# Kernel optimization log

Measured on AMD Instinct MI355X. Metric: run time of the kernel, lower is better.

Reference implementation:

```python
import jax, jax.numpy as jnp
import numpy as np

B, S, T, D = 4, 2, 1024, 512
H = 8
HD = D // H
EPS = 1e-6
LN_EPS = 1e-5


def setup_inputs() -> dict:
    key = jax.random.key(0)
    ks = jax.random.split(key, 12)
    def lin(k, fan_in, shape):
        bound = 1.0 / np.sqrt(fan_in)
        return jax.random.uniform(k, shape, jnp.float32, -bound, bound)
    return {
        "hidden_states": jax.random.normal(ks[0], (B, S, T, D), jnp.float32),
        "Wq": lin(ks[1], D, (D, D)), "bq": lin(ks[2], D, (D,)),
        "Wk": lin(ks[3], D, (D, D)), "bk": lin(ks[4], D, (D,)),
        "Wv": lin(ks[5], D, (D, D)), "bv": lin(ks[6], D, (D,)),
        "Wo": lin(ks[7], D, (D, D)), "bo": lin(ks[8], D, (D,)),
        "ln_g": jnp.ones((S, D), jnp.float32),
        "ln_b": jnp.zeros((S, D), jnp.float32),
        "gate_alpha": jnp.full((S,), 0.01, jnp.float32),
    }


def _heads(x):
    # [B,T,D] -> [B,H,T,HD]
    return x.reshape(B, T, H, HD).transpose(0, 2, 1, 3)


def _layernorm(x, g, b):
    mu = jnp.mean(x, axis=-1, keepdims=True)
    var = jnp.var(x, axis=-1, keepdims=True)
    return (x - mu) * jax.lax.rsqrt(var + LN_EPS) * g + b


def reference(hidden_states, Wq, bq, Wk, bk, Wv, bv, Wo, bo, ln_g, ln_b, gate_alpha):
    h1, h2 = hidden_states[:, 0], hidden_states[:, 1]  # [B,T,D]
    proj = lambda x, W, b: jnp.einsum('btd,ed->bte', x, W) + b
    Q1, K1, V1 = _heads(proj(h1, Wq, bq)), _heads(proj(h1, Wk, bk)), _heads(proj(h1, Wv, bv))
    Q2, K2, V2 = _heads(proj(h2, Wq, bq)), _heads(proj(h2, Wk, bk)), _heads(proj(h2, Wv, bv))
    scale = 1.0 / np.sqrt(HD)
    L12 = jnp.einsum('bhqd,bhkd->bhqk', Q1, K2) * scale
    L21 = jnp.einsum('bhqd,bhkd->bhqk', Q2, K1) * scale
    S12 = jax.nn.softmax(L12, axis=-1)
    S21 = jax.nn.softmax(L21, axis=-1)
    M = S12 + S21 + EPS
    A12 = S12 / M
    A21 = S21 / M
    H1 = jnp.einsum('bhqk,bhkd->bhqd', A12, V2).transpose(0, 2, 1, 3).reshape(B, T, D)
    H2 = jnp.einsum('bhqk,bhkd->bhqd', A21, V1).transpose(0, 2, 1, 3).reshape(B, T, D)
    H1 = _layernorm(jnp.einsum('btd,ed->bte', H1, Wo) + bo, ln_g[0], ln_b[0])
    H2 = _layernorm(jnp.einsum('btd,ed->bte', H2, Wo) + bo, ln_g[1], ln_b[1])
    attn = jnp.stack([H1, H2], axis=1)  # [B,2,T,D]
    return hidden_states + attn * gate_alpha[None, :, None, None]
```

## Files before the change

### kernel.cpp

```cpp
#include <hip/hip_runtime.h>

#define DEVI __device__ __forceinline__

typedef __bf16 v8bf __attribute__((ext_vector_type(8)));
typedef float  v4f  __attribute__((ext_vector_type(4)));
typedef short  v4s  __attribute__((ext_vector_type(4)));

DEVI unsigned short f2bf(float f) {
  unsigned u = __builtin_bit_cast(unsigned, f);
  u += 0x7fffu + ((u >> 16) & 1u);
  return (unsigned short)(u >> 16);
}
DEVI v4f MFMA32(v8bf a, v8bf b, v4f c) {
  return __builtin_amdgcn_mfma_f32_16x16x32_bf16(a, b, c, 0, 0, 0);
}
DEVI v8bf ldfrag(const unsigned short* p) {
  return __builtin_bit_cast(v8bf, *(const uint4*)p);
}
DEVI v4s ld4s(const unsigned short* p) {
  return __builtin_bit_cast(v4s, *(const uint2*)p);
}
DEVI unsigned pkbf(float lo, float hi) {
  unsigned a = __builtin_bit_cast(unsigned, hi) + 0x8000u;
  unsigned b = __builtin_bit_cast(unsigned, lo) + 0x8000u;
  return __builtin_amdgcn_perm(a, b, 0x07060302u);
}
DEVI float lo2f(unsigned u) { return __builtin_bit_cast(float, u << 16); }
DEVI float hi2f(unsigned u) { return __builtin_bit_cast(float, u & 0xffff0000u); }

DEVI void drain_vmem() { asm volatile("s_waitcnt vmcnt(0)" ::: "memory"); }

#if __has_builtin(__builtin_amdgcn_exp2f)
DEVI float fexp2(float x) { return __builtin_amdgcn_exp2f(x); }
#else
DEVI float fexp2(float x) { return exp2f(x); }
#endif

#if __has_builtin(__builtin_amdgcn_mfma_f32_16x16x16bf16_1k)
#define HAVE_MFMA16 1
DEVI v4f MFMA16(v4s a, v4s b, v4f c) {
  return __builtin_amdgcn_mfma_f32_16x16x16bf16_1k(a, b, c, 0, 0, 0);
}
#else
#define HAVE_MFMA16 0
#endif

#if __has_builtin(__builtin_amdgcn_global_load_lds)
DEVI void g2l(const unsigned short* g, unsigned short* l) {
  __builtin_amdgcn_global_load_lds(
      (const __attribute__((address_space(1))) unsigned int*)g,
      (__attribute__((address_space(3))) unsigned int*)l, 16, 0, 0);
}
#else
DEVI void g2l(const unsigned short* g, unsigned short* l) {
  *(uint4*)((char*)l + (threadIdx.x & 63) * 16) = *(const uint4*)g;
}
#endif

__global__ __launch_bounds__(256) void convert_kernel(
    const float* __restrict__ X, const float* __restrict__ Wq,
    const float* __restrict__ Wk, const float* __restrict__ Wv,
    const float* __restrict__ Wo, unsigned short* __restrict__ dst)
{
  int t = blockIdx.x * 256 + threadIdx.x;
  int idx = t * 4;
  const float* src;
  if (idx < 4194304) {
    src = X + idx;
  } else {
    int u = idx - 4194304;
    int w = u >> 18;
    const float* W = (w == 0) ? Wq : (w == 1) ? Wk : (w == 2) ? Wv : Wo;
    src = W + (u & 262143);
  }
  float4 f = *(const float4*)src;
  uint2 o;
  o.x = pkbf(f.x, f.y);
  o.y = pkbf(f.z, f.w);
  *(uint2*)&dst[idx] = o;
}

template<int OUTM, int BM>
__global__ __launch_bounds__(256) void gemm_bt(
    const unsigned short* __restrict__ A,
    const unsigned short* __restrict__ W0, const unsigned short* __restrict__ W1,
    const unsigned short* __restrict__ W2,
    const float* __restrict__ b0, const float* __restrict__ b1, const float* __restrict__ b2,
    void* __restrict__ C0, void* __restrict__ C1, void* __restrict__ C2)
{
  const int K = 512, N = 512;
  const int MI = BM / 32;
  const int PER = (BM / 8 + 16) / 4;
  __shared__ unsigned short sAB[2][(BM + 128) * 64];

  const int gx = gridDim.x, gy = gridDim.y;
  const int nwg = gx * gy * gridDim.z;
  const int lin = (blockIdx.z * gy + blockIdx.y) * gx + blockIdx.x;
  const int wsw = (lin & 7) * (nwg >> 3) + (lin >> 3);
  const int bx = wsw % gx, by = (wsw / gx) % gy;
  const int z = wsw / (gx * gy);

  const unsigned short* W = (z == 0) ? W0 : (z == 1) ? W1 : W2;
  const float* bias = (z == 0) ? b0 : (z == 1) ? b1 : b2;
  void* C = (z == 0) ? C0 : (z == 1) ? C1 : C2;

  const int tid = threadIdx.x;
  const int lane = tid & 63, wave = tid >> 6;
  const int l15 = lane & 15, quad = lane >> 4, swl = l15 & 7;
  const int lrow = lane >> 3;
  const int lc8 = ((lane & 7) ^ (lrow & 7)) * 8;
  const int wm = (wave >> 1) * (BM / 2), wn = (wave & 1) * 64;
  const int mbase = by * BM, nbase = bx * 128;

  const unsigned short* gsrc[PER];
  int loff[PER];
#pragma unroll
  for (int t = 0; t < PER; t++) {
    int c = wave * PER + t;
    loff[t] = c * 512;
    if (c < BM / 8) gsrc[t] = A + (size_t)(mbase + c * 8 + lrow) * K + lc8;
    else            gsrc[t] = W + (size_t)(nbase + (c - BM / 8) * 8 + lrow) * K + lc8;
  }

  v4f acc[MI][4] = {};

#pragma unroll
  for (int t = 0; t < PER; t++) g2l(gsrc[t], &sAB[0][loff[t]]);

  for (int kt = 0; kt < K / 64; kt++) {
    drain_vmem();
    __syncthreads();
    if (kt < K / 64 - 1) {
#pragma unroll
      for (int t = 0; t < PER; t++)
        g2l(gsrc[t] + (kt + 1) * 64, &sAB[(kt + 1) & 1][loff[t]]);
    }
    const int bu = kt & 1;
#pragma unroll
    for (int s = 0; s < 2; s++) {
      v8bf af[MI], bf[4];
#pragma unroll
      for (int i = 0; i < MI; i++)
        af[i] = ldfrag(&sAB[bu][(wm + i * 16 + l15) * 64 + ((s * 4 + quad) ^ swl) * 8]);
#pragma unroll
      for (int j = 0; j < 4; j++)
        bf[j] = ldfrag(&sAB[bu][(BM + wn + j * 16 + l15) * 64 + ((s * 4 + quad) ^ swl) * 8]);
#pragma unroll
      for (int i = 0; i < MI; i++)
#pragma unroll
        for (int j = 0; j < 4; j++)
          acc[i][j] = MFMA32(af[i], bf[j], acc[i][j]);
    }
  }

  if (OUTM == 0 && BM == 128 && z == 2) {
    const int TP = 136;
    unsigned short* T = &sAB[0][0];
    __syncthreads();
#pragma unroll
    for (int i = 0; i < MI; i++)
#pragma unroll
      for (int j = 0; j < 4; j++) {
        int tp = wm + i * 16 + quad * 4;
        int c  = wn + j * 16 + l15;
        int col = nbase + c;
        float v[4];
#pragma unroll
        for (int r = 0; r < 4; r++) v[r] = acc[i][j][r] + bias[col];
        uint2 o;
        o.x = pkbf(v[0], v[1]);
        o.y = pkbf(v[2], v[3]);
        *(uint2*)&T[c * TP + tp] = o;
      }
    __syncthreads();
    const int bs = mbase >> 10, tbase = mbase & 1023;
    const int hh0 = nbase >> 6;
#pragma unroll
    for (int it = 0; it < 8; it++) {
      int rh = wave * 32 + it * 4 + quad;
      uint4 d = *(const uint4*)&T[rh * TP + l15 * 8];
      int rowIdx = (bs * 8 + hh0 + (rh >> 6)) * 64 + (rh & 63);
      *(uint4*)&((unsigned short*)C)[(size_t)rowIdx * 1024 + tbase + l15 * 8] = d;
    }
  } else {
#pragma unroll
    for (int i = 0; i < MI; i++)
#pragma unroll
      for (int j = 0; j < 4; j++) {
        int row0 = mbase + wm + i * 16 + quad * 4;
        int col = nbase + wn + j * 16 + l15;
        float v[4];
#pragma unroll
        for (int r = 0; r < 4; r++) v[r] = acc[i][j][r] + bias[col];
        if (OUTM == 1) {
#pragma unroll
          for (int r = 0; r < 4; r++) ((float*)C)[(size_t)(row0 + r) * N + col] = v[r];
        } else if (z == 2) {
          int bs = row0 >> 10, t0 = row0 & 1023;
          int hh = col >> 6, hd = col & 63;
          uint2 o;
          o.x = pkbf(v[0], v[1]);
          o.y = pkbf(v[2], v[3]);
          *(uint2*)&((unsigned short*)C)[(size_t)((bs * 8 + hh) * 64 + hd) * 1024 + t0] = o;
        } else {
#pragma unroll
          for (int r = 0; r < 4; r++)
            ((unsigned short*)C)[(size_t)(row0 + r) * N + col] = f2bf(v[r]);
        }
      }
  }
}

__global__ __launch_bounds__(256, 4) void attn_a(
    const unsigned short* __restrict__ Qg, const unsigned short* __restrict__ Kg,
    float* __restrict__ Lws)
{
  __shared__ unsigned short sK[2][2][64][64];

  const int pair = blockIdx.x & 31;
  const int b = pair >> 3, h = pair & 7;
  const int qt = (blockIdx.x >> 5) & 15;
  const int kh = blockIdx.x >> 9;
  const int tid = threadIdx.x;
  const int lane = tid & 63, wave = tid >> 6;
  const int l15 = lane & 15, quad = lane >> 4, swl = l15 & 7;
  const int lrow = lane >> 3;
  const int lc8 = ((lane & 7) ^ (lrow & 7)) * 8;
  const int qbase = qt * 64 + wave * 16;
  const float S2 = 0.125f * 1.44269504f;

  const unsigned short* kgp[2];
#pragma unroll
  for (int st = 0; st < 2; st++)
    kgp[st] = Kg + (size_t)((b * 2 + st) * 1024) * 512 + h * 64;

  v8bf qf[2][2];
#pragma unroll
  for (int d = 0; d < 2; d++)
#pragma unroll
    for (int s = 0; s < 2; s++) {
      int qrow = (b * 2 + d) * 1024 + qbase + l15;
      qf[d][s] = ldfrag(&Qg[(size_t)qrow * 512 + h * 64 + s * 32 + quad * 8]);
    }

  const unsigned short* gA[4];
  unsigned short* lA[2][4];
#pragma unroll
  for (int t = 0; t < 4; t++) {
    int c = wave * 4 + t;
    gA[t] = kgp[c >> 3] + (size_t)((c & 7) * 8 + lrow) * 512 + lc8
            + (size_t)kh * 262144;
    lA[0][t] = &sK[0][c >> 3][(c & 7) * 8][0];
    lA[1][t] = &sK[1][c >> 3][(c & 7) * 8][0];
  }

  float lacc[2] = {0.f, 0.f};
#pragma unroll
  for (int t = 0; t < 4; t++) g2l(gA[t], lA[0][t]);

  for (int kt = 0; kt < 8; kt++) {
    drain_vmem();
    __syncthreads();
    if (kt < 7) {
#pragma unroll
      for (int t = 0; t < 4; t++)
        g2l(gA[t] + (size_t)(kt + 1) * 32768, lA[(kt + 1) & 1][t]);
    }
    const int bu = kt & 1;
    v4f acc[2][4] = {};
#pragma unroll
    for (int s = 0; s < 2; s++)
#pragma unroll
      for (int d = 0; d < 2; d++)
#pragma unroll
        for (int j = 0; j < 4; j++) {
          v8bf kf = ldfrag(&sK[bu][1 - d][j * 16 + l15][((s * 4 + quad) ^ swl) * 8]);
          acc[d][j] = MFMA32(kf, qf[d][s], acc[d][j]);
        }
#pragma unroll
    for (int d = 0; d < 2; d++)
#pragma unroll
      for (int j = 0; j < 4; j++)
#pragma unroll
        for (int r = 0; r < 4; r++)
          lacc[d] += fexp2(acc[d][j][r] * S2);
  }

  float lv[2];
#pragma unroll
  for (int d = 0; d < 2; d++) {
    float v = lacc[d];
    v += __shfl_xor(v, 16);
    v += __shfl_xor(v, 32);
    lv[d] = v;
  }
  if (quad == 0) {
#pragma unroll
    for (int d = 0; d < 2; d++) {
      int qrow = (b * 2 + d) * 1024 + qbase + l15;
      Lws[(size_t)qrow * 2 + kh] = lv[d];
    }
  }
}

__global__ __launch_bounds__(256, 2) void attn_b(
    const unsigned short* __restrict__ Qg, const unsigned short* __restrict__ Kg,
    const unsigned short* __restrict__ VTg, const float* __restrict__ Lws,
    unsigned short* __restrict__ Hc)
{
  __shared__ unsigned short sK[2][2][64][64];
  __shared__ unsigned short sV[2][2][64][64];

  const int pair = blockIdx.x & 31;
  const int b = pair >> 3, h = pair & 7;
  const int qt = blockIdx.x >> 5;
  const int tid = threadIdx.x;
  const int lane = tid & 63, wave = tid >> 6;
  const int l15 = lane & 15, quad = lane >> 4, swl = l15 & 7;
  const int lrow = lane >> 3;
  const int lc8 = ((lane & 7) ^ (lrow & 7)) * 8;
  const int qbase = qt * 64 + wave * 16;
  const float S2 = 0.125f * 1.44269504f;

  const unsigned short* kgp[2];
  const unsigned short* vgp[2];
#pragma unroll
  for (int st = 0; st < 2; st++) {
    kgp[st] = Kg + (size_t)((b * 2 + st) * 1024) * 512 + h * 64;
    vgp[st] = VTg + (size_t)(((b * 2 + st) * 8 + h) * 64) * 1024;
  }

  v8bf qf[2][2];
#pragma unroll
  for (int d = 0; d < 2; d++)
#pragma unroll
    for (int s = 0; s < 2; s++) {
      int qrow = (b * 2 + d) * 1024 + qbase + l15;
      qf[d][s] = ldfrag(&Qg[(size_t)qrow * 512 + h * 64 + s * 32 + quad * 8]);
    }

  float ll[2];
#pragma unroll
  for (int d = 0; d < 2; d++) {
    int qrow = (b * 2 + d) * 1024 + qbase + l15;
    float2 p = *(const float2*)&Lws[(size_t)qrow * 2];
    ll[d] = __log2f(p.x + p.y);
  }
  const float dll = ll[0] - ll[1];

  v4f oacc[2][4] = {};
  {
    const unsigned short* gB[8];
    unsigned short* lB[2][8];
    size_t stp[8];
#pragma unroll
    for (int t = 0; t < 8; t++) {
      int c = wave * 8 + t;
      if (c < 16) {
        gB[t] = kgp[c >> 3] + (size_t)((c & 7) * 8 + lrow) * 512 + lc8;
        stp[t] = 32768;
        lB[0][t] = &sK[0][c >> 3][(c & 7) * 8][0];
        lB[1][t] = &sK[1][c >> 3][(c & 7) * 8][0];
      } else {
        int cv = c - 16;
        gB[t] = vgp[cv >> 3] + (size_t)((cv & 7) * 8 + lrow) * 1024 + lc8;
        stp[t] = 64;
        lB[0][t] = &sV[0][cv >> 3][(cv & 7) * 8][0];
        lB[1][t] = &sV[1][cv >> 3][(cv & 7) * 8][0];
      }
    }
#pragma unroll
    for (int t = 0; t < 8; t++) g2l(gB[t], lB[0][t]);

    for (int kt = 0; kt < 16; kt++) {
      drain_vmem();
      __syncthreads();
      if (kt < 15) {
#pragma unroll
        for (int t = 0; t < 8; t++)
          g2l(gB[t] + (size_t)(kt + 1) * stp[t], lB[(kt + 1) & 1][t]);
      }
      const int bu = kt & 1;

      v4f acc[2][4] = {};
#pragma unroll
      for (int s = 0; s < 2; s++)
#pragma unroll
        for (int d = 0; d < 2; d++)
#pragma unroll
          for (int j = 0; j < 4; j++) {
            v8bf kf = ldfrag(&sK[bu][1 - d][j * 16 + l15][((s * 4 + quad) ^ swl) * 8]);
            acc[d][j] = MFMA32(kf, qf[d][s], acc[d][j]);
          }

#pragma unroll
      for (int j = 0; j < 4; j++) {
        float r0[4], r1[4];
#pragma unroll
        for (int r = 0; r < 4; r++) {
          float t = fmaf(acc[1][j][r] - acc[0][j][r], S2, dll);
          float ri = __builtin_amdgcn_rcpf(1.f + fexp2(t));
          r0[r] = ri;
          r1[r] = 1.f - ri;
        }
#if HAVE_MFMA16
        uint2 w0, w1;
        w0.x = pkbf(r0[0], r0[1]); w0.y = pkbf(r0[2], r0[3]);
        w1.x = pkbf(r1[0], r1[1]); w1.y = pkbf(r1[2], r1[3]);
        v4s af0 = __builtin_bit_cast(v4s, w0);
        v4s af1 = __builtin_bit_cast(v4s, w1);
        int vcol = ((j * 2 + (quad >> 1)) ^ swl) * 8 + (quad & 1) * 4;
#pragma unroll
        for (int nt = 0; nt < 4; nt++) {
          v4s vf0 = ld4s(&sV[bu][1][nt * 16 + l15][vcol]);
          v4s vf1 = ld4s(&sV[bu][0][nt * 16 + l15][vcol]);
          oacc[0][nt] = MFMA16(af0, vf0, oacc[0][nt]);
          oacc[1][nt] = MFMA16(af1, vf1, oacc[1][nt]);
        }
#else
#pragma unroll
        for (int d = 0; d < 2; d++) {
          float (&cb)[4] = (d == 0) ? r0 : r1;
          v8bf a;
#pragma unroll
          for (int jj = 0; jj < 8; jj++) {
            int src = l15 + 16 * ((jj >> 2) + (quad & 1) * 2);
            float v = __shfl(cb[jj & 3], src);
            a[jj] = __builtin_bit_cast(__bf16, f2bf(v));
          }
#pragma unroll
          for (int nt = 0; nt < 4; nt++) {
            v8bf vf = ldfrag(&sV[bu][1 - d][nt * 16 + l15]
                               [(((j & 2) * 2 + quad) ^ swl) * 8]);
            oacc[d][nt] = MFMA32(a, vf, oacc[d][nt]);
          }
        }
#endif
      }
    }
  }

#pragma unroll
  for (int d = 0; d < 2; d++)
#pragma unroll
    for (int nt = 0; nt < 4; nt++)
#pragma unroll
      for (int r = 0; r < 4; r++) {
        int row = (b * 2 + d) * 1024 + qbase + quad * 4 + r;
        int col = h * 64 + nt * 16 + l15;
        Hc[(size_t)row * 512 + col] = f2bf(oacc[d][nt][r]);
      }
}

__global__ __launch_bounds__(256) void ln_kernel(
    const unsigned short* __restrict__ Pb, const float* __restrict__ hidden,
    const float* __restrict__ ln_g, const float* __restrict__ ln_b,
    const float* __restrict__ gate, float* __restrict__ out)
{
  const int row = blockIdx.x * 4 + (threadIdx.x >> 6);
  const int s = (row >> 10) & 1;
  const int lane = threadIdx.x & 63;
  const int d0 = lane * 8;

  uint4 up = *(const uint4*)&Pb[(size_t)row * 512 + d0];
  float x[8] = { lo2f(up.x), hi2f(up.x), lo2f(up.y), hi2f(up.y),
                 lo2f(up.z), hi2f(up.z), lo2f(up.w), hi2f(up.w) };
  float s1 = 0.f, s2 = 0.f;
#pragma unroll
  for (int i = 0; i < 8; i++) { s1 += x[i]; s2 += x[i] * x[i]; }
#pragma unroll
  for (int m = 1; m < 64; m <<= 1) { s1 += __shfl_xor(s1, m); s2 += __shfl_xor(s2, m); }
  float mu = s1 * (1.f / 512.f);
  float var = s2 * (1.f / 512.f) - mu * mu;
  float rs = rsqrtf(var + 1e-5f);
  float al = gate[s];

  float4 h0 = *(const float4*)&hidden[(size_t)row * 512 + d0];
  float4 h1 = *(const float4*)&hidden[(size_t)row * 512 + d0 + 4];
  float4 g0 = *(const float4*)&ln_g[s * 512 + d0];
  float4 g1 = *(const float4*)&ln_g[s * 512 + d0 + 4];
  float4 bb0 = *(const float4*)&ln_b[s * 512 + d0];
  float4 bb1 = *(const float4*)&ln_b[s * 512 + d0 + 4];
  float4 o0, o1;
  o0.x = h0.x + ((x[0] - mu) * rs * g0.x + bb0.x) * al;
  o0.y = h0.y + ((x[1] - mu) * rs * g0.y + bb0.y) * al;
  o0.z = h0.z + ((x[2] - mu) * rs * g0.z + bb0.z) * al;
  o0.w = h0.w + ((x[3] - mu) * rs * g0.w + bb0.w) * al;
  o1.x = h1.x + ((x[4] - mu) * rs * g1.x + bb1.x) * al;
  o1.y = h1.y + ((x[5] - mu) * rs * g1.y + bb1.y) * al;
  o1.z = h1.z + ((x[6] - mu) * rs * g1.z + bb1.z) * al;
  o1.w = h1.w + ((x[7] - mu) * rs * g1.w + bb1.w) * al;
  *(float4*)&out[(size_t)row * 512 + d0] = o0;
  *(float4*)&out[(size_t)row * 512 + d0 + 4] = o1;
}

extern "C" void kernel_launch(void* const* d_in, const int* in_sizes, int n_in,
                              void* d_out, int out_size, void* d_ws, size_t ws_size,
                              hipStream_t stream)
{
  const float* hidden = (const float*)d_in[0];
  const float* Wq = (const float*)d_in[1];
  const float* bq = (const float*)d_in[2];
  const float* Wk = (const float*)d_in[3];
  const float* bk = (const float*)d_in[4];
  const float* Wv = (const float*)d_in[5];
  const float* bv = (const float*)d_in[6];
  const float* Wo = (const float*)d_in[7];
  const float* bo = (const float*)d_in[8];
  const float* ln_g = (const float*)d_in[9];
  const float* ln_b = (const float*)d_in[10];
  const float* gate = (const float*)d_in[11];

  unsigned short* U = (unsigned short*)d_ws;
  unsigned short* Xbf = U;
  unsigned short* Wqb = U + 4194304;
  unsigned short* Wkb = U + 4456448;
  unsigned short* Wvb = U + 4718592;
  unsigned short* Wob = U + 4980736;
  unsigned short* Qg  = U + 5242880;
  unsigned short* Kg  = U + 9437184;
  unsigned short* VT  = U + 13631488;
  unsigned short* Hc  = U + 17825792;
  unsigned short* Pb  = (unsigned short*)((char*)d_ws + 44302336);
  float* Lws = (float*)d_ws;

  convert_kernel<<<dim3(5120), 256, 0, stream>>>(hidden, Wq, Wk, Wv, Wo, Xbf);
  gemm_bt<0, 128><<<dim3(4, 64, 3), 256, 0, stream>>>(Xbf, Wqb, Wkb, Wvb, bq, bk, bv, Qg, Kg, VT);
  attn_a<<<dim3(1024), 256, 0, stream>>>(Qg, Kg, Lws);
  attn_b<<<dim3(512), 256, 0, stream>>>(Qg, Kg, VT, Lws, Hc);
  gemm_bt<0, 64><<<dim3(4, 128, 1), 256, 0, stream>>>(Hc, Wob, Wob, Wob, bo, bo, bo, Pb, Pb, Pb);
  ln_kernel<<<dim3(2048), 256, 0, stream>>>(Pb, hidden, ln_g, ln_b, gate, (float*)d_out);
}
```

Before: 172.6 us.

## Fuse fp32-to-bf16 activation conversion into QKV GEMM loads; add MFMA priority hints

Drops the separate bf16 conversion pass over the hidden states. The QKV GEMM now reads fp32 activations straight into registers, converts them, and writes them to LDS, while the weight tiles keep using the async global-to-LDS path. This removes a 16 MB read plus an 8 MB write and round trip through memory. The cost is register-staged loads done by only two waves, a heavier wait that also drains LDS traffic, and 2x the A-tile global read bytes inside the GEMM. s_setprio hints are also added around the MFMA sections in the attention kernels.

New measurement: 175.4 us. No clear change (+1.6%).

```diff
diff --git a/kernel.cpp b/kernel.cpp
--- a/kernel.cpp
+++ b/kernel.cpp
@@ -29,6 +29,7 @@
 DEVI float hi2f(unsigned u) { return __builtin_bit_cast(float, u & 0xffff0000u); }
 
 DEVI void drain_vmem() { asm volatile("s_waitcnt vmcnt(0)" ::: "memory"); }
+DEVI void drain_all()  { asm volatile("s_waitcnt vmcnt(0) lgkmcnt(0)" ::: "memory"); }
 
 #if __has_builtin(__builtin_amdgcn_exp2f)
 DEVI float fexp2(float x) { return __builtin_amdgcn_exp2f(x); }
@@ -58,31 +59,24 @@
 #endif
 
 __global__ __launch_bounds__(256) void convert_kernel(
-    const float* __restrict__ X, const float* __restrict__ Wq,
-    const float* __restrict__ Wk, const float* __restrict__ Wv,
-    const float* __restrict__ Wo, unsigned short* __restrict__ dst)
+    const float* __restrict__ Wq, const float* __restrict__ Wk,
+    const float* __restrict__ Wv, const float* __restrict__ Wo,
+    unsigned short* __restrict__ dst)
 {
   int t = blockIdx.x * 256 + threadIdx.x;
   int idx = t * 4;
-  const float* src;
-  if (idx < 4194304) {
-    src = X + idx;
-  } else {
-    int u = idx - 4194304;
-    int w = u >> 18;
-    const float* W = (w == 0) ? Wq : (w == 1) ? Wk : (w == 2) ? Wv : Wo;
-    src = W + (u & 262143);
-  }
-  float4 f = *(const float4*)src;
+  int w = idx >> 18;
+  const float* W = (w == 0) ? Wq : (w == 1) ? Wk : (w == 2) ? Wv : Wo;
+  float4 f = *(const float4*)(W + (idx & 262143));
   uint2 o;
   o.x = pkbf(f.x, f.y);
   o.y = pkbf(f.z, f.w);
   *(uint2*)&dst[idx] = o;
 }
 
-template<int OUTM, int BM>
+template<int OUTM, int BM, int AF32>
 __global__ __launch_bounds__(256) void gemm_bt(
-    const unsigned short* __restrict__ A,
+    const void* __restrict__ Ain,
     const unsigned short* __restrict__ W0, const unsigned short* __restrict__ W1,
     const unsigned short* __restrict__ W2,
     const float* __restrict__ b0, const float* __restrict__ b1, const float* __restrict__ b2,
@@ -113,27 +107,69 @@
   const int mbase = by * BM, nbase = bx * 128;
 
   const unsigned short* gsrc[PER];
+  const float* fsrc[PER];
   int loff[PER];
 #pragma unroll
   for (int t = 0; t < PER; t++) {
     int c = wave * PER + t;
     loff[t] = c * 512;
-    if (c < BM / 8) gsrc[t] = A + (size_t)(mbase + c * 8 + lrow) * K + lc8;
-    else            gsrc[t] = W + (size_t)(nbase + (c - BM / 8) * 8 + lrow) * K + lc8;
+    if (c < BM / 8) {
+      if constexpr (AF32)
+        fsrc[t] = (const float*)Ain + (size_t)(mbase + c * 8 + lrow) * K + lc8;
+      else
+        gsrc[t] = (const unsigned short*)Ain + (size_t)(mbase + c * 8 + lrow) * K + lc8;
+    } else {
+      gsrc[t] = W + (size_t)(nbase + (c - BM / 8) * 8 + lrow) * K + lc8;
+    }
   }
 
   v4f acc[MI][4] = {};
-
-#pragma unroll
-  for (int t = 0; t < PER; t++) g2l(gsrc[t], &sAB[0][loff[t]]);
+  float4 pfa[PER], pfb[PER];
+
+  if constexpr (AF32) {
+    if (wave < 2) {
+#pragma unroll
+      for (int t = 0; t < PER; t++) {
+        pfa[t] = *(const float4*)fsrc[t];
+        pfb[t] = *(const float4*)(fsrc[t] + 4);
+      }
+#pragma unroll
+      for (int t = 0; t < PER; t++) {
+        uint4 o;
+        o.x = pkbf(pfa[t].x, pfa[t].y); o.y = pkbf(pfa[t].z, pfa[t].w);
+        o.z = pkbf(pfb[t].x, pfb[t].y); o.w = pkbf(pfb[t].z, pfb[t].w);
+        *(uint4*)(&sAB[0][loff[t]] + lane * 8) = o;
+      }
+    } else {
+#pragma unroll
+      for (int t = 0; t < PER; t++) g2l(gsrc[t], &sAB[0][loff[t]]);
+    }
+  } else {
+#pragma unroll
+    for (int t = 0; t < PER; t++) g2l(gsrc[t], &sAB[0][loff[t]]);
+  }
 
   for (int kt = 0; kt < K / 64; kt++) {
-    drain_vmem();
+    if constexpr (AF32) drain_all(); else drain_vmem();
     __syncthreads();
     if (kt < K / 64 - 1) {
-#pragma unroll
-      for (int t = 0; t < PER; t++)
-        g2l(gsrc[t] + (kt + 1) * 64, &sAB[(kt + 1) & 1][loff[t]]);
+      if constexpr (AF32) {
+        if (wave < 2) {
+#pragma unroll
+          for (int t = 0; t < PER; t++) {
+            pfa[t] = *(const float4*)(fsrc[t] + (kt + 1) * 64);
+            pfb[t] = *(const float4*)(fsrc[t] + (kt + 1) * 64 + 4);
+          }
+        } else {
+#pragma unroll
+          for (int t = 0; t < PER; t++)
+            g2l(gsrc[t] + (kt + 1) * 64, &sAB[(kt + 1) & 1][loff[t]]);
+        }
+      } else {
+#pragma unroll
+        for (int t = 0; t < PER; t++)
+          g2l(gsrc[t] + (kt + 1) * 64, &sAB[(kt + 1) & 1][loff[t]]);
+      }
     }
     const int bu = kt & 1;
 #pragma unroll
@@ -150,6 +186,17 @@
 #pragma unroll
         for (int j = 0; j < 4; j++)
           acc[i][j] = MFMA32(af[i], bf[j], acc[i][j]);
+    }
+    if constexpr (AF32) {
+      if (wave < 2 && kt < K / 64 - 1) {
+#pragma unroll
+        for (int t = 0; t < PER; t++) {
+          uint4 o;
+          o.x = pkbf(pfa[t].x, pfa[t].y); o.y = pkbf(pfa[t].z, pfa[t].w);
+          o.z = pkbf(pfb[t].x, pfb[t].y); o.w = pkbf(pfb[t].z, pfb[t].w);
+          *(uint4*)(&sAB[(kt + 1) & 1][loff[t]] + lane * 8) = o;
+        }
+      }
     }
   }
 
@@ -268,6 +315,7 @@
     }
     const int bu = kt & 1;
     v4f acc[2][4] = {};
+    __builtin_amdgcn_s_setprio(1);
 #pragma unroll
     for (int s = 0; s < 2; s++)
 #pragma unroll
@@ -277,6 +325,7 @@
           v8bf kf = ldfrag(&sK[bu][1 - d][j * 16 + l15][((s * 4 + quad) ^ swl) * 8]);
           acc[d][j] = MFMA32(kf, qf[d][s], acc[d][j]);
         }
+    __builtin_amdgcn_s_setprio(0);
 #pragma unroll
     for (int d = 0; d < 2; d++)
 #pragma unroll
@@ -383,6 +432,7 @@
       const int bu = kt & 1;
 
       v4f acc[2][4] = {};
+      __builtin_amdgcn_s_setprio(1);
 #pragma unroll
       for (int s = 0; s < 2; s++)
 #pragma unroll
@@ -392,6 +442,7 @@
             v8bf kf = ldfrag(&sK[bu][1 - d][j * 16 + l15][((s * 4 + quad) ^ swl) * 8]);
             acc[d][j] = MFMA32(kf, qf[d][s], acc[d][j]);
           }
+      __builtin_amdgcn_s_setprio(0);
 
 #pragma unroll
       for (int j = 0; j < 4; j++) {
@@ -410,6 +461,7 @@
         v4s af0 = __builtin_bit_cast(v4s, w0);
         v4s af1 = __builtin_bit_cast(v4s, w1);
         int vcol = ((j * 2 + (quad >> 1)) ^ swl) * 8 + (quad & 1) * 4;
+        __builtin_amdgcn_s_setprio(1);
 #pragma unroll
         for (int nt = 0; nt < 4; nt++) {
           v4s vf0 = ld4s(&sV[bu][1][nt * 16 + l15][vcol]);
@@ -417,6 +469,7 @@
           oacc[0][nt] = MFMA16(af0, vf0, oacc[0][nt]);
           oacc[1][nt] = MFMA16(af1, vf1, oacc[1][nt]);
         }
+        __builtin_amdgcn_s_setprio(0);
 #else
 #pragma unroll
         for (int d = 0; d < 2; d++) {
@@ -512,7 +565,6 @@
   const float* gate = (const float*)d_in[11];
 
   unsigned short* U = (unsigned short*)d_ws;
-  unsigned short* Xbf = U;
   unsigned short* Wqb = U + 4194304;
   unsigned short* Wkb = U + 4456448;
   unsigned short* Wvb = U + 4718592;
@@ -524,10 +576,10 @@
   unsigned short* Pb  = (unsigned short*)((char*)d_ws + 44302336);
   float* Lws = (float*)d_ws;
 
-  convert_kernel<<<dim3(5120), 256, 0, stream>>>(hidden, Wq, Wk, Wv, Wo, Xbf);
-  gemm_bt<0, 128><<<dim3(4, 64, 3), 256, 0, stream>>>(Xbf, Wqb, Wkb, Wvb, bq, bk, bv, Qg, Kg, VT);
+  convert_kernel<<<dim3(1024), 256, 0, stream>>>(Wq, Wk, Wv, Wo, Wqb);
+  gemm_bt<0, 128, 1><<<dim3(4, 64, 3), 256, 0, stream>>>(hidden, Wqb, Wkb, Wvb, bq, bk, bv, Qg, Kg, VT);
   attn_a<<<dim3(1024), 256, 0, stream>>>(Qg, Kg, Lws);
   attn_b<<<dim3(512), 256, 0, stream>>>(Qg, Kg, VT, Lws, Hc);
-  gemm_bt<0, 64><<<dim3(4, 128, 1), 256, 0, stream>>>(Hc, Wob, Wob, Wob, bo, bo, bo, Pb, Pb, Pb);
+  gemm_bt<0, 64, 0><<<dim3(4, 128, 1), 256, 0, stream>>>(Hc, Wob, Wob, Wob, bo, bo, bo, Pb, Pb, Pb);
   ln_kernel<<<dim3(2048), 256, 0, stream>>>(Pb, hidden, ln_g, ln_b, gate, (float*)d_out);
 }
```
